# Optimization experiments

Measured on AMD Instinct MI355X. Metric: run time of the kernel, lower is better.

Reference implementation:

```python
import jax, jax.numpy as jnp
import numpy as np

B = 16384
N_DENSE = 13
N_TABLES = 26
V = 1000000
E = 2  # embedding dim (hard-coded in source)


def setup_inputs() -> dict:
    key = jax.random.key(0)
    ks = jax.random.split(key, 12)
    x_dense = jax.random.normal(ks[0], (B, N_DENSE), dtype=jnp.float32)
    x_cat = jax.random.randint(ks[1], (B, N_TABLES), 0, V, dtype=jnp.int64)
    # All tables share the same num_embeddings, so stack into one [T, V, E] array.
    emb = jax.random.normal(ks[2], (N_TABLES, V, E), dtype=jnp.float32) * 0.05
    # bottom MLP: 13 -> 3 -> 2
    bot_w1 = jax.random.normal(ks[3], (N_DENSE, 3), dtype=jnp.float32) * 0.1
    bot_b1 = jnp.zeros((3,), dtype=jnp.float32)
    bot_w2 = jax.random.normal(ks[4], (3, 2), dtype=jnp.float32) * 0.1
    bot_b2 = jnp.zeros((2,), dtype=jnp.float32)
    # top MLP: 54 -> 4 -> 2 -> 1
    top_w1 = jax.random.normal(ks[5], (E * N_TABLES + 2, 4), dtype=jnp.float32) * 0.1
    top_b1 = jnp.zeros((4,), dtype=jnp.float32)
    top_w2 = jax.random.normal(ks[6], (4, 2), dtype=jnp.float32) * 0.1
    top_b2 = jnp.zeros((2,), dtype=jnp.float32)
    top_w3 = jax.random.normal(ks[7], (2, 1), dtype=jnp.float32) * 0.1
    top_b3 = jnp.zeros((1,), dtype=jnp.float32)
    return {
        "x_dense": x_dense, "x_cat": x_cat, "emb": emb,
        "bot_w1": bot_w1, "bot_b1": bot_b1, "bot_w2": bot_w2, "bot_b2": bot_b2,
        "top_w1": top_w1, "top_b1": top_b1, "top_w2": top_w2, "top_b2": top_b2,
        "top_w3": top_w3, "top_b3": top_b3,
    }


def reference(x_dense, x_cat, emb, bot_w1, bot_b1, bot_w2, bot_b2,
              top_w1, top_b1, top_w2, top_b2, top_w3, top_b3):
    # bottom MLP on dense features: [B,13] -> [B,2]
    d = jax.nn.relu(x_dense @ bot_w1 + bot_b1)
    d = jax.nn.relu(d @ bot_w2 + bot_b2)
    # multi-table embedding gather: emb[t, x_cat[:, t]] -> [B, T, E]
    table_idx = jnp.arange(N_TABLES)[None, :]  # [1, T]
    e = emb[table_idx, x_cat]                  # [B, T, E]
    e = e.reshape(e.shape[0], N_TABLES * E)    # [B, 52]
    x = jnp.concatenate([d, e], axis=1)        # [B, 54]
    # top MLP: 54 -> 4 -> 2 -> 1 with sigmoid
    h = jax.nn.relu(x @ top_w1 + top_b1)
    h = jax.nn.relu(h @ top_w2 + top_b2)
    out = jax.nn.sigmoid(h @ top_w3 + top_b3)
    return out
```

## Files before the change

kernel.cpp:

```cpp
#include <hip/hip_runtime.h>
#include <math.h>

#define B_TOTAL   16384
#define N_DENSE   13
#define N_TABLES  26
#define V_ROWS    1000000
#define E_DIM     2

__global__ __launch_bounds__(64) void dlrm_fused_kernel(
    const float* __restrict__ x_dense,
    const int*   __restrict__ x_cat,
    const float* __restrict__ emb,
    const float* __restrict__ bw1,
    const float* __restrict__ bb1,
    const float* __restrict__ bw2,
    const float* __restrict__ bb2,
    const float* __restrict__ tw1,
    const float* __restrict__ tb1,
    const float* __restrict__ tw2,
    const float* __restrict__ tb2,
    const float* __restrict__ tw3,
    const float* __restrict__ tb3,
    float*       __restrict__ out)
{
    const int b = blockIdx.x * blockDim.x + threadIdx.x;
    if (b >= B_TOTAL) return;

    float ev[2 * N_TABLES];
    {
        const long long cbase = (long long)b * N_TABLES;
        #pragma unroll
        for (int t = 0; t < N_TABLES; ++t) {
            const int idx = x_cat[cbase + t];
            const float2 v = *reinterpret_cast<const float2*>(
                emb + ((size_t)t * V_ROWS + (size_t)idx) * E_DIM);
            ev[2 * t]     = v.x;
            ev[2 * t + 1] = v.y;
        }
    }

    float xd[N_DENSE];
    {
        const long long dbase = (long long)b * N_DENSE;
        #pragma unroll
        for (int i = 0; i < N_DENSE; ++i) xd[i] = x_dense[dbase + i];
    }
    float d1[3];
    #pragma unroll
    for (int j = 0; j < 3; ++j) {
        float acc = bb1[j];
        #pragma unroll
        for (int i = 0; i < N_DENSE; ++i) acc = fmaf(xd[i], bw1[i * 3 + j], acc);
        d1[j] = fmaxf(acc, 0.0f);
    }
    float d2[2];
    #pragma unroll
    for (int j = 0; j < 2; ++j) {
        float acc = bb2[j];
        #pragma unroll
        for (int i = 0; i < 3; ++i) acc = fmaf(d1[i], bw2[i * 2 + j], acc);
        d2[j] = fmaxf(acc, 0.0f);
    }

    float h1[4];
    #pragma unroll
    for (int j = 0; j < 4; ++j) {
        float acc = tb1[j];
        acc = fmaf(d2[0], tw1[0 * 4 + j], acc);
        acc = fmaf(d2[1], tw1[1 * 4 + j], acc);
        #pragma unroll
        for (int i = 0; i < 2 * N_TABLES; ++i)
            acc = fmaf(ev[i], tw1[(2 + i) * 4 + j], acc);
        h1[j] = fmaxf(acc, 0.0f);
    }
    float h2[2];
    #pragma unroll
    for (int j = 0; j < 2; ++j) {
        float acc = tb2[j];
        #pragma unroll
        for (int i = 0; i < 4; ++i) acc = fmaf(h1[i], tw2[i * 2 + j], acc);
        h2[j] = fmaxf(acc, 0.0f);
    }
    float z = tb3[0];
    z = fmaf(h2[0], tw3[0], z);
    z = fmaf(h2[1], tw3[1], z);

    out[b] = 1.0f / (1.0f + expf(-z));
}

extern "C" void kernel_launch(void* const* d_in, const int* in_sizes, int n_in,
                              void* d_out, int out_size, void* d_ws, size_t ws_size,
                              hipStream_t stream) {
    const float* x_dense = (const float*)d_in[0];
    const int*   x_cat   = (const int*)  d_in[1];
    const float* emb     = (const float*)d_in[2];
    const float* bw1     = (const float*)d_in[3];
    const float* bb1     = (const float*)d_in[4];
    const float* bw2     = (const float*)d_in[5];
    const float* bb2     = (const float*)d_in[6];
    const float* tw1     = (const float*)d_in[7];
    const float* tb1     = (const float*)d_in[8];
    const float* tw2     = (const float*)d_in[9];
    const float* tb2     = (const float*)d_in[10];
    const float* tw3     = (const float*)d_in[11];
    const float* tb3     = (const float*)d_in[12];
    float* out = (float*)d_out;

    const int block = 64;
    const int grid  = (B_TOTAL + block - 1) / block;
    dlrm_fused_kernel<<<grid, block, 0, stream>>>(
        x_dense, x_cat, emb, bw1, bb1, bw2, bb2,
        tw1, tb1, tw2, tb2, tw3, tb3, out);
}
```

Before: 272.9 us.

## Split each sample's embedding gathers across four lanes with shuffle reduction

Each batch sample is now handled by four adjacent threads. Each thread gathers an interleaved subset of the 26 tables and computes a partial first-layer top-MLP sum, and the partials are combined with xor shuffles. This gives four times as many threads for the random gathers, which should raise memory-level parallelism and occupancy. In exchange, the bottom MLP and later layers run redundantly in all four lanes, the dense inputs are read four times, and there is extra shuffle overhead.

```diff
diff --git a/kernel.cpp b/kernel.cpp
--- a/kernel.cpp
+++ b/kernel.cpp
@@ -6,6 +6,7 @@
 #define N_TABLES  26
 #define V_ROWS    1000000
 #define E_DIM     2
+#define SPLIT     4
 
 __global__ __launch_bounds__(64) void dlrm_fused_kernel(
     const float* __restrict__ x_dense,
@@ -23,28 +24,32 @@
     const float* __restrict__ tb3,
     float*       __restrict__ out)
 {
-    const int b = blockIdx.x * blockDim.x + threadIdx.x;
+    const int gtid = blockIdx.x * blockDim.x + threadIdx.x;
+    const int b = gtid >> 2;
+    const int r = gtid & 3;
     if (b >= B_TOTAL) return;
 
-    float ev[2 * N_TABLES];
-    {
-        const long long cbase = (long long)b * N_TABLES;
-        #pragma unroll
-        for (int t = 0; t < N_TABLES; ++t) {
-            const int idx = x_cat[cbase + t];
-            const float2 v = *reinterpret_cast<const float2*>(
-                emb + ((size_t)t * V_ROWS + (size_t)idx) * E_DIM);
-            ev[2 * t]     = v.x;
-            ev[2 * t + 1] = v.y;
-        }
+    const int cbase = b * N_TABLES;
+    float2 ev[6];
+    #pragma unroll
+    for (int k = 0; k < 6; ++k) {
+        const int t   = r + 4 * k;
+        const int idx = x_cat[cbase + t];
+        ev[k] = *reinterpret_cast<const float2*>(
+            emb + ((size_t)t * V_ROWS + (size_t)idx) * E_DIM);
+    }
+    const int t6 = 24 + r;
+    float2 ev6 = make_float2(0.0f, 0.0f);
+    if (r < 2) {
+        const int idx = x_cat[cbase + t6];
+        ev6 = *reinterpret_cast<const float2*>(
+            emb + ((size_t)t6 * V_ROWS + (size_t)idx) * E_DIM);
     }
 
     float xd[N_DENSE];
-    {
-        const long long dbase = (long long)b * N_DENSE;
-        #pragma unroll
-        for (int i = 0; i < N_DENSE; ++i) xd[i] = x_dense[dbase + i];
-    }
+    const int dbase = b * N_DENSE;
+    #pragma unroll
+    for (int i = 0; i < N_DENSE; ++i) xd[i] = x_dense[dbase + i];
     float d1[3];
     #pragma unroll
     for (int j = 0; j < 3; ++j) {
@@ -62,15 +67,36 @@
         d2[j] = fmaxf(acc, 0.0f);
     }
 
+    float h1p[4] = {0.0f, 0.0f, 0.0f, 0.0f};
+    #pragma unroll
+    for (int k = 0; k < 6; ++k) {
+        const int t = r + 4 * k;
+        #pragma unroll
+        for (int j = 0; j < 4; ++j) {
+            h1p[j] = fmaf(ev[k].x, tw1[(2 + 2 * t) * 4 + j], h1p[j]);
+            h1p[j] = fmaf(ev[k].y, tw1[(3 + 2 * t) * 4 + j], h1p[j]);
+        }
+    }
+    if (r < 2) {
+        #pragma unroll
+        for (int j = 0; j < 4; ++j) {
+            h1p[j] = fmaf(ev6.x, tw1[(2 + 2 * t6) * 4 + j], h1p[j]);
+            h1p[j] = fmaf(ev6.y, tw1[(3 + 2 * t6) * 4 + j], h1p[j]);
+        }
+    }
+
+    #pragma unroll
+    for (int j = 0; j < 4; ++j) {
+        h1p[j] += __shfl_xor(h1p[j], 1);
+        h1p[j] += __shfl_xor(h1p[j], 2);
+    }
+
     float h1[4];
     #pragma unroll
     for (int j = 0; j < 4; ++j) {
-        float acc = tb1[j];
+        float acc = tb1[j] + h1p[j];
         acc = fmaf(d2[0], tw1[0 * 4 + j], acc);
         acc = fmaf(d2[1], tw1[1 * 4 + j], acc);
-        #pragma unroll
-        for (int i = 0; i < 2 * N_TABLES; ++i)
-            acc = fmaf(ev[i], tw1[(2 + i) * 4 + j], acc);
         h1[j] = fmaxf(acc, 0.0f);
     }
     float h2[2];
@@ -85,7 +111,7 @@
     z = fmaf(h2[0], tw3[0], z);
     z = fmaf(h2[1], tw3[1], z);
 
-    out[b] = 1.0f / (1.0f + expf(-z));
+    if (r == 0) out[b] = 1.0f / (1.0f + expf(-z));
 }
 
 extern "C" void kernel_launch(void* const* d_in, const int* in_sizes, int n_in,
@@ -107,7 +133,7 @@
     float* out = (float*)d_out;
 
     const int block = 64;
-    const int grid  = (B_TOTAL + block - 1) / block;
+    const int grid  = (B_TOTAL * SPLIT + block - 1) / block;
     dlrm_fused_kernel<<<grid, block, 0, stream>>>(
         x_dense, x_cat, emb, bw1, bb1, bw2, bb2,
         tw1, tb1, tw2, tb2, tw3, tb3, out);
```

After: 275.2 us. No clear change (+0.8%).
